# Kernel tuning notes

Measured on AMD Instinct MI355X. Metric: run time of the kernel, lower is better.

The kernel has to match this reference:

```python
import jax, jax.numpy as jnp
import numpy as np

B, C, H, Wd = 4096, 32, 14, 14
ENC_DIM = 512
ATT_DIM = 128


def setup_inputs() -> dict:
    key = jax.random.key(0)
    ks = jax.random.split(key, 10)
    s = 0.05
    return {
        "img_features": jax.random.normal(ks[0], (B, C, H, Wd), jnp.float32),
        "prev_hidden": jax.random.normal(ks[1], (B, ENC_DIM), jnp.float32),
        "W_w": jax.random.normal(ks[2], (ATT_DIM, C), jnp.float32) * s,
        "W_b": jnp.zeros((ATT_DIM,), jnp.float32),
        "U_w": jax.random.normal(ks[3], (ATT_DIM, ENC_DIM), jnp.float32) * s,
        "U_b": jnp.zeros((ATT_DIM,), jnp.float32),
        "v_w": jax.random.normal(ks[4], (1, ATT_DIM), jnp.float32) * s,
        "v_b": jnp.zeros((1,), jnp.float32),
        "fb_w": jax.random.normal(ks[5], (C, ENC_DIM), jnp.float32) * s,
        "fb_b": jnp.zeros((C,), jnp.float32),
    }


def reference(img_features, prev_hidden, W_w, W_b, U_w, U_b, v_w, v_b, fb_w, fb_b):
    b = img_features.shape[0]
    c = img_features.shape[1]
    # [B, C, H, W] -> [B, P, C] where P = H*W (spatial positions)
    img_parts = img_features.reshape(b, c, -1).transpose(0, 2, 1)
    W_s = jnp.einsum('bpc,ac->bpa', img_parts, W_w) + W_b          # [B, P, 128]
    U_h = prev_hidden @ U_w.T + U_b                                 # [B, 128]
    att = jnp.tanh(W_s + U_h[:, None, :])                           # [B, P, 128]
    score = jnp.einsum('bpa,a->bp', att, v_w[0]) + v_b[0]           # [B, P]
    att_weights = jax.nn.softmax(score, axis=1)                     # softmax over spatial
    context = jnp.einsum('bpc,bp->bc', img_parts, att_weights)      # [B, 32]
    beta = jax.nn.sigmoid(prev_hidden @ fb_w.T + fb_b)              # [B, 32]
    context = context * beta
    return (context, att_weights)
```

## Files before the change

kernel.cpp:

```cpp
#include <hip/hip_runtime.h>
#include <hip/hip_bf16.h>


typedef __attribute__((ext_vector_type(8))) short short8;
typedef __attribute__((ext_vector_type(8))) __bf16 bf16x8;
typedef __attribute__((ext_vector_type(4))) float floatx4;
typedef __attribute__((ext_vector_type(4))) unsigned int uint4v;

#define K2E 2.8853900817779268f

#if __has_builtin(__builtin_amdgcn_exp2f)
#define EXP2F(x) __builtin_amdgcn_exp2f(x)
#else
#define EXP2F(x) __expf(0.6931471805599453f * (x))
#endif

static __device__ __forceinline__ float bf2f(unsigned short u) {
    union { unsigned int i; float f; } v; v.i = ((unsigned int)u) << 16; return v.f;
}
static __device__ __forceinline__ unsigned short f2bf(float f) {
    union { float f; unsigned int i; } v; v.f = f;
    unsigned int r = v.i + 0x7FFFu + ((v.i >> 16) & 1u);
    return (unsigned short)(r >> 16);
}
static __device__ __forceinline__ float sigmoid_rcp(float x) {
    return __builtin_amdgcn_rcpf(1.0f + __expf(-x));
}
static __device__ __forceinline__ void split_trunc8(const float* src, bf16x8* hi, bf16x8* lo) {
    uint4v u0 = *(const uint4v*)src;
    uint4v u1 = *(const uint4v*)(src + 4);
    unsigned int fb[8], lb[8];
#pragma unroll
    for (int j = 0; j < 4; j++) { fb[j] = u0[j]; fb[4 + j] = u1[j]; }
#pragma unroll
    for (int k = 0; k < 8; k++) {
        float x = __uint_as_float(fb[k]);
        float h = __uint_as_float(fb[k] & 0xFFFF0000u);
        lb[k] = __float_as_uint(x - h);
    }
    uint4v hp, lp;
#pragma unroll
    for (int j = 0; j < 4; j++) {
        hp[j] = __builtin_amdgcn_perm(fb[2 * j + 1], fb[2 * j], 0x07060302u);
        lp[j] = __builtin_amdgcn_perm(lb[2 * j + 1], lb[2 * j], 0x07060302u);
    }
    *hi = __builtin_bit_cast(bf16x8, hp);
    *lo = __builtin_bit_cast(bf16x8, lp);
}

__global__ __launch_bounds__(256) void k0_split(
    const float* __restrict__ U_w, const float* __restrict__ fb_w,
    const float* __restrict__ W_w,
    unsigned short* __restrict__ Bhi, unsigned short* __restrict__ Blo,
    unsigned short* __restrict__ Whi)
{
    int i = blockIdx.x * 256 + threadIdx.x;
    if (i < 81920) {
        float x = (i < 65536) ? U_w[i] : fb_w[i - 65536];
        unsigned short h = f2bf(x);
        Bhi[i] = h;
        Blo[i] = f2bf(x - bf2f(h));
    } else {
        Whi[i - 81920] = f2bf(W_w[i - 81920] * K2E);
    }
}

__global__ __launch_bounds__(256) void k1_gemm(
    const float* __restrict__ hidden,
    const unsigned short* __restrict__ Bhi, const unsigned short* __restrict__ Blo,
    const float* __restrict__ U_b, const float* __restrict__ W_b,
    const float* __restrict__ fb_b,
    float* __restrict__ uh_out, float* __restrict__ beta_out,
    float* __restrict__ partial, int nsplit, int direct)
{
    __shared__ float s_part[4 * 2560];
    const int tid = threadIdx.x;
    const int wave = tid >> 6, lane = tid & 63, quad = lane >> 4, l16 = lane & 15;
    const int mtile = blockIdx.x / nsplit;
    const int kblock = 512 / nsplit;
    const int ks0 = (blockIdx.x % nsplit) * kblock + wave * (kblock >> 2);
    const int ksteps = kblock >> 7;
    const int arow = mtile * 16 + l16;

    floatx4 acc[10];
#pragma unroll
    for (int i = 0; i < 10; i++) acc[i] = (floatx4)(0.0f);

    for (int ksi = 0; ksi < ksteps; ksi++) {
        const int e0 = ks0 + ksi * 32 + quad * 8;
        bf16x8 ah, al;
        split_trunc8(hidden + (size_t)arow * 512 + e0, &ah, &al);
#pragma unroll
        for (int n = 0; n < 10; n++) {
            const size_t bo = (size_t)(n * 16 + l16) * 512 + e0;
            bf16x8 bh = *(const bf16x8*)(Bhi + bo);
            bf16x8 bl = *(const bf16x8*)(Blo + bo);
            acc[n] = __builtin_amdgcn_mfma_f32_16x16x32_bf16(ah, bl, acc[n], 0, 0, 0);
            acc[n] = __builtin_amdgcn_mfma_f32_16x16x32_bf16(al, bh, acc[n], 0, 0, 0);
            acc[n] = __builtin_amdgcn_mfma_f32_16x16x32_bf16(ah, bh, acc[n], 0, 0, 0);
        }
    }
#pragma unroll
    for (int n = 0; n < 10; n++)
#pragma unroll
        for (int r = 0; r < 4; r++)
            s_part[wave * 2560 + (quad * 4 + r) * 160 + n * 16 + l16] = acc[n][r];
    __syncthreads();

#pragma unroll
    for (int j = 0; j < 10; j++) {
        const int i = tid + j * 256;
        float v = s_part[i] + s_part[2560 + i] + s_part[5120 + i] + s_part[7680 + i];
        if (direct) {
            const int m = mtile * 16 + i / 160, col = i % 160;
            if (col < 128) uh_out[(size_t)m * 128 + col] = K2E * (v + U_b[col] + W_b[col]);
            else beta_out[(size_t)m * 32 + (col - 128)] = sigmoid_rcp(v + fb_b[col - 128]);
        } else {
            partial[(size_t)blockIdx.x * 2560 + i] = v;
        }
    }
}

__global__ __launch_bounds__(256) void k1b_reduce(
    const float* __restrict__ partial,
    const float* __restrict__ U_b, const float* __restrict__ W_b,
    const float* __restrict__ fb_b,
    float* __restrict__ uh_out, float* __restrict__ beta_out, int nsplit)
{
    const int idx = blockIdx.x * 256 + threadIdx.x;
    const int mt = idx / 2560, r = idx % 2560;
    float v = 0.0f;
    for (int s = 0; s < nsplit; s++)
        v += partial[(size_t)(mt * nsplit + s) * 2560 + r];
    const int m = mt * 16 + r / 160, col = r % 160;
    if (col < 128) uh_out[(size_t)m * 128 + col] = K2E * (v + U_b[col] + W_b[col]);
    else beta_out[(size_t)m * 32 + (col - 128)] = sigmoid_rcp(v + fb_b[col - 128]);
}

#define HSTR 40

__global__ __launch_bounds__(256, 4) void k2_attn(
    const float* __restrict__ img,
    const unsigned short* __restrict__ Whi,
    const float* __restrict__ v_w,
    const float* __restrict__ uh,
    const float* __restrict__ beta,
    float* __restrict__ out)
{
    __shared__ __align__(16) unsigned short s_imgh[208 * HSTR];
    __shared__ float s_score[208];
    __shared__ float s_red[4];
    __shared__ float s_ctx[4][32];

    const int tid = threadIdx.x;
    const int b = blockIdx.x;
    const int wave = tid >> 6, lane = tid & 63, quad = lane >> 4, l16 = lane & 15;

    if (tid < 196) {
        const size_t base = (size_t)b * 6272 + tid;
#pragma unroll
        for (int g = 0; g < 4; g++) {
            unsigned int hb[8];
#pragma unroll
            for (int j = 0; j < 8; j++) {
                unsigned int u = __float_as_uint(img[base + (size_t)(8 * g + j) * 196]);
                hb[j] = u + 0x7FFFu + ((u >> 16) & 1u);
            }
            uint4v hp;
#pragma unroll
            for (int j = 0; j < 4; j++)
                hp[j] = __builtin_amdgcn_perm(hb[2 * j + 1], hb[2 * j], 0x07060302u);
            *(uint4v*)&s_imgh[tid * HSTR + g * 8] = hp;
        }
    } else {
        for (int i = tid - 196; i < 12 * HSTR; i += 60) s_imgh[196 * HSTR + i] = 0;
        if (tid < 208) s_score[tid] = 0.0f;
    }

    float uaR[8], va2R[8], sv = 0.0f;
#pragma unroll
    for (int nt = 0; nt < 8; nt++) {
        uaR[nt] = uh[(size_t)b * 128 + nt * 16 + l16];
        float v = v_w[nt * 16 + l16];
        sv += v;
        va2R[nt] = -2.0f * v;
    }
    sv += __shfl_xor(sv, 1); sv += __shfl_xor(sv, 2);
    sv += __shfl_xor(sv, 4); sv += __shfl_xor(sv, 8);
    __syncthreads();

    float esum = 0.0f;
    for (int mt = wave; mt < 13; mt += 4) {
        bf16x8 a = *(const bf16x8*)&s_imgh[(mt * 16 + l16) * HSTR + quad * 8];
        float sc4[4] = {0.f, 0.f, 0.f, 0.f};
#pragma unroll
        for (int nt = 0; nt < 8; nt++) {
            bf16x8 bh = *(const bf16x8*)(Whi + (nt * 16 + l16) * 32 + quad * 8);
            const float ua = uaR[nt];
            floatx4 d = {ua, ua, ua, ua};
            d = __builtin_amdgcn_mfma_f32_16x16x32_bf16(a, bh, d, 0, 0, 0);
#pragma unroll
            for (int r = 0; r < 4; r++) {
                float e = EXP2F(d[r]);
                float rr = __builtin_amdgcn_rcpf(1.0f + e);
                sc4[r] = __builtin_fmaf(va2R[nt], rr, sc4[r]);
            }
        }
#pragma unroll
        for (int r = 0; r < 4; r++) {
            float s = sc4[r];
            s += __shfl_xor(s, 1); s += __shfl_xor(s, 2);
            s += __shfl_xor(s, 4); s += __shfl_xor(s, 8);
            const int p = mt * 16 + quad * 4 + r;
            if (l16 == 0 && p < 196) {
                float e = __expf(sv + s);
                s_score[p] = e;
                esum += e;
            }
        }
    }
    esum += __shfl_xor(esum, 16);
    esum += __shfl_xor(esum, 32);
    if (lane == 0) s_red[wave] = esum;
    __syncthreads();

    const float tot = s_red[0] + s_red[1] + s_red[2] + s_red[3];
    const float rtot = __builtin_amdgcn_rcpf(tot);
    if (tid < 196)
        out[131072 + (size_t)b * 196 + tid] = s_score[tid] * rtot;

    {
        const int c = lane & 31;
        const int po = wave * 2 + (lane >> 5);
        float acc = 0.0f;
#pragma unroll 5
        for (int j = 0; j < 25; j++) {
            const int p = po + j * 8;
            acc = __builtin_fmaf(bf2f(s_imgh[p * HSTR + c]), s_score[p], acc);
        }
        acc += __shfl_xor(acc, 32);
        if ((lane >> 5) == 0) s_ctx[wave][c] = acc;
    }
    __syncthreads();
    if (tid < 32) {
        const float v = s_ctx[0][tid] + s_ctx[1][tid] + s_ctx[2][tid] + s_ctx[3][tid];
        out[(size_t)b * 32 + tid] = v * rtot * beta[(size_t)b * 32 + tid];
    }
}

extern "C" void kernel_launch(void* const* d_in, const int* in_sizes, int n_in,
                              void* d_out, int out_size, void* d_ws, size_t ws_size,
                              hipStream_t stream) {
    const float* img    = (const float*)d_in[0];
    const float* hidden = (const float*)d_in[1];
    const float* W_w    = (const float*)d_in[2];
    const float* W_b    = (const float*)d_in[3];
    const float* U_w    = (const float*)d_in[4];
    const float* U_b    = (const float*)d_in[5];
    const float* v_w    = (const float*)d_in[6];
    const float* fb_w   = (const float*)d_in[8];
    const float* fb_b   = (const float*)d_in[9];
    float* out = (float*)d_out;

    float* uh_ws   = (float*)d_ws;
    float* beta_ws = uh_ws + 4096 * 128;
    unsigned short* Bhi = (unsigned short*)(beta_ws + 4096 * 32);
    unsigned short* Blo = Bhi + 81920;
    unsigned short* Whi = Blo + 81920;
    float* partial = (float*)(Whi + 4096);
    const size_t fixed_bytes = ((char*)partial) - ((char*)d_ws);

    int nsplit = 1, direct = 1;
    if (ws_size >= fixed_bytes + (size_t)256 * 4 * 2560 * 4) { nsplit = 4; direct = 0; }
    else if (ws_size >= fixed_bytes + (size_t)256 * 2 * 2560 * 4) { nsplit = 2; direct = 0; }
    else if (ws_size >= fixed_bytes + (size_t)256 * 1 * 2560 * 4) { nsplit = 1; direct = 0; }

    k0_split<<<dim3(336), dim3(256), 0, stream>>>(U_w, fb_w, W_w, Bhi, Blo, Whi);
    k1_gemm<<<dim3(256 * nsplit), dim3(256), 0, stream>>>(
        hidden, Bhi, Blo, U_b, W_b, fb_b, uh_ws, beta_ws, partial, nsplit, direct);
    if (!direct)
        k1b_reduce<<<dim3(2560), dim3(256), 0, stream>>>(
            partial, U_b, W_b, fb_b, uh_ws, beta_ws, nsplit);
    k2_attn<<<dim3(4096), dim3(256), 0, stream>>>(img, Whi, v_w, uh_ws, beta_ws, out);
}
```

Baseline: 204.7 us.

## Give each GEMM wave its own M-tile and widen attention loads and context reduction

The projection GEMM now assigns each of the four waves a separate 16-row M-tile over the full K slice, instead of splitting K across waves. This removes the shared-memory cross-wave reduction and its barrier, but launches a quarter as many blocks. The attention kernel now issues 16 image loads at once before the bf16 packing, so more memory requests are in flight. The context reduction reads bf16 pairs and processes two channels per lane with shuffle reductions, giving fewer LDS reads per output.

```diff
diff --git a/kernel.cpp b/kernel.cpp
--- a/kernel.cpp
+++ b/kernel.cpp
@@ -73,13 +73,14 @@
     float* __restrict__ uh_out, float* __restrict__ beta_out,
     float* __restrict__ partial, int nsplit, int direct)
 {
-    __shared__ float s_part[4 * 2560];
     const int tid = threadIdx.x;
     const int wave = tid >> 6, lane = tid & 63, quad = lane >> 4, l16 = lane & 15;
-    const int mtile = blockIdx.x / nsplit;
+    const int mgroup = blockIdx.x / nsplit;
+    const int s = blockIdx.x % nsplit;
+    const int mtile = mgroup * 4 + wave;
     const int kblock = 512 / nsplit;
-    const int ks0 = (blockIdx.x % nsplit) * kblock + wave * (kblock >> 2);
-    const int ksteps = kblock >> 7;
+    const int ks0 = s * kblock;
+    const int ksteps = kblock >> 5;
     const int arow = mtile * 16 + l16;
 
     floatx4 acc[10];
@@ -100,23 +101,23 @@
             acc[n] = __builtin_amdgcn_mfma_f32_16x16x32_bf16(ah, bh, acc[n], 0, 0, 0);
         }
     }
-#pragma unroll
-    for (int n = 0; n < 10; n++)
-#pragma unroll
-        for (int r = 0; r < 4; r++)
-            s_part[wave * 2560 + (quad * 4 + r) * 160 + n * 16 + l16] = acc[n][r];
-    __syncthreads();
-
-#pragma unroll
-    for (int j = 0; j < 10; j++) {
-        const int i = tid + j * 256;
-        float v = s_part[i] + s_part[2560 + i] + s_part[5120 + i] + s_part[7680 + i];
-        if (direct) {
-            const int m = mtile * 16 + i / 160, col = i % 160;
-            if (col < 128) uh_out[(size_t)m * 128 + col] = K2E * (v + U_b[col] + W_b[col]);
-            else beta_out[(size_t)m * 32 + (col - 128)] = sigmoid_rcp(v + fb_b[col - 128]);
-        } else {
-            partial[(size_t)blockIdx.x * 2560 + i] = v;
+
+#pragma unroll
+    for (int n = 0; n < 10; n++) {
+        const int col = n * 16 + l16;
+#pragma unroll
+        for (int r = 0; r < 4; r++) {
+            if (direct) {
+                const int m = mtile * 16 + quad * 4 + r;
+                if (col < 128)
+                    uh_out[(size_t)m * 128 + col] = K2E * (acc[n][r] + U_b[col] + W_b[col]);
+                else
+                    beta_out[(size_t)m * 32 + (col - 128)] =
+                        sigmoid_rcp(acc[n][r] + fb_b[col - 128]);
+            } else {
+                partial[(size_t)(mtile * nsplit + s) * 2560 + (quad * 4 + r) * 160 + col]
+                    = acc[n][r];
+            }
         }
     }
 }
@@ -157,20 +158,26 @@
     const int wave = tid >> 6, lane = tid & 63, quad = lane >> 4, l16 = lane & 15;
 
     if (tid < 196) {
-        const size_t base = (size_t)b * 6272 + tid;
-#pragma unroll
-        for (int g = 0; g < 4; g++) {
-            unsigned int hb[8];
-#pragma unroll
-            for (int j = 0; j < 8; j++) {
-                unsigned int u = __float_as_uint(img[base + (size_t)(8 * g + j) * 196]);
+        const float* src = img + (size_t)b * 6272 + tid;
+#pragma unroll
+        for (int h = 0; h < 2; h++) {
+            float v[16];
+#pragma unroll
+            for (int j = 0; j < 16; j++) v[j] = src[(size_t)(h * 16 + j) * 196];
+            unsigned int hb[16];
+#pragma unroll
+            for (int j = 0; j < 16; j++) {
+                unsigned int u = __float_as_uint(v[j]);
                 hb[j] = u + 0x7FFFu + ((u >> 16) & 1u);
             }
-            uint4v hp;
-#pragma unroll
-            for (int j = 0; j < 4; j++)
-                hp[j] = __builtin_amdgcn_perm(hb[2 * j + 1], hb[2 * j], 0x07060302u);
-            *(uint4v*)&s_imgh[tid * HSTR + g * 8] = hp;
+            uint4v hp0, hp1;
+#pragma unroll
+            for (int j = 0; j < 4; j++) {
+                hp0[j] = __builtin_amdgcn_perm(hb[2 * j + 1], hb[2 * j], 0x07060302u);
+                hp1[j] = __builtin_amdgcn_perm(hb[8 + 2 * j + 1], hb[8 + 2 * j], 0x07060302u);
+            }
+            *(uint4v*)&s_imgh[tid * HSTR + h * 16] = hp0;
+            *(uint4v*)&s_imgh[tid * HSTR + h * 16 + 8] = hp1;
         }
     } else {
         for (int i = tid - 196; i < 12 * HSTR; i += 60) s_imgh[196 * HSTR + i] = 0;
@@ -230,16 +237,23 @@
         out[131072 + (size_t)b * 196 + tid] = s_score[tid] * rtot;
 
     {
-        const int c = lane & 31;
-        const int po = wave * 2 + (lane >> 5);
-        float acc = 0.0f;
-#pragma unroll 5
-        for (int j = 0; j < 25; j++) {
-            const int p = po + j * 8;
-            acc = __builtin_fmaf(bf2f(s_imgh[p * HSTR + c]), s_score[p], acc);
-        }
-        acc += __shfl_xor(acc, 32);
-        if ((lane >> 5) == 0) s_ctx[wave][c] = acc;
+        const int c2 = (lane & 15) * 2;
+        const int po = wave * 4 + (lane >> 4);
+        float a0 = 0.0f, a1 = 0.0f;
+#pragma unroll
+        for (int j = 0; j < 13; j++) {
+            const int p = po + j * 16;
+            const unsigned int pair = *(const unsigned int*)&s_imgh[p * HSTR + c2];
+            const float w = s_score[p];
+            a0 = __builtin_fmaf(bf2f((unsigned short)(pair & 0xFFFFu)), w, a0);
+            a1 = __builtin_fmaf(bf2f((unsigned short)(pair >> 16)), w, a1);
+        }
+        a0 += __shfl_xor(a0, 16); a0 += __shfl_xor(a0, 32);
+        a1 += __shfl_xor(a1, 16); a1 += __shfl_xor(a1, 32);
+        if (lane < 16) {
+            s_ctx[wave][c2] = a0;
+            s_ctx[wave][c2 + 1] = a1;
+        }
     }
     __syncthreads();
     if (tid < 32) {
@@ -276,7 +290,7 @@
     else if (ws_size >= fixed_bytes + (size_t)256 * 1 * 2560 * 4) { nsplit = 1; direct = 0; }
 
     k0_split<<<dim3(336), dim3(256), 0, stream>>>(U_w, fb_w, W_w, Bhi, Blo, Whi);
-    k1_gemm<<<dim3(256 * nsplit), dim3(256), 0, stream>>>(
+    k1_gemm<<<dim3(64 * nsplit), dim3(256), 0, stream>>>(
         hidden, Bhi, Blo, U_b, W_b, fb_b, uh_ws, beta_ws, partial, nsplit, direct);
     if (!direct)
         k1b_reduce<<<dim3(2560), dim3(256), 0, stream>>>(
```

Measured after the change: 207.7 us. Within noise of the previous version (+1.5%).
